# Kernel tuning notes

Hardware: AMD Instinct MI355X
Metric: run time of the kernel (lower is better)

Reference implementation:

```python
import jax, jax.numpy as jnp
import numpy as np

EPS = 1e-12  # matches torch F.normalize eps


def _l2_normalize(x):
    n = jnp.linalg.norm(x, axis=-1, keepdims=True)
    return x / jnp.maximum(n, EPS)


def setup_inputs() -> dict:
    key = jax.random.key(0)
    k1, k2, k3 = jax.random.split(key, 3)
    N, E, D = 100000, 1200000, 64
    feat = jax.random.normal(k1, (N, D), dtype=jnp.float32)
    beta = jnp.ones((1,), dtype=jnp.float32)
    src = jax.random.randint(k2, (E,), 0, N, dtype=jnp.int32)
    dst = jax.random.randint(k3, (E,), 0, N, dtype=jnp.int32)
    return {"feat": feat, "beta": beta, "src": src, "dst": dst}


def reference(feat, beta, src, dst):
    N = feat.shape[0]
    # cosine similarity on each edge (AGNN att_type)
    nh = _l2_normalize(feat)                                  # [N, D]
    e = beta[0] * jnp.sum(nh[src] * nh[dst], axis=-1)         # [E]
    # edge softmax over incoming edges of each destination node
    emax = jax.ops.segment_max(e, dst, num_segments=N)        # [N]
    emax = jnp.where(jnp.isfinite(emax), emax, 0.0)           # isolated nodes
    p = jnp.exp(e - emax[dst])                                # [E]
    psum = jax.ops.segment_sum(p, dst, num_segments=N)        # [N]
    p = p / jnp.maximum(psum[dst], EPS)                       # [E]
    # weighted scatter-sum aggregation: h_i' = sum_j p_ij * h_j
    msg = feat[src] * p[:, None]                              # [E, D]
    out = jax.ops.segment_sum(msg, dst, num_segments=N)       # [N, D]
    return out
```

## Files before the change

### kernel.cpp

```cpp
#include <hip/hip_runtime.h>
#include <hip/hip_fp16.h>

#define D 64
#define EPS 1e-12f
#define NPB 512
#define NPB_SHIFT 9
#define NB 256
#define CAP 8192
#define CAP_SHIFT 13
#define EPB 4096
#define SRC_BITS 17

typedef _Float16 hv2 __attribute__((ext_vector_type(2)));

__device__ inline unsigned bc_u(__half2 h) { return __builtin_bit_cast(unsigned, h); }
__device__ inline __half2  bc_h(unsigned u) { return __builtin_bit_cast(__half2, u); }

__device__ inline float fdot2f(unsigned a, unsigned b, float c) {
#if defined(__has_builtin) && __has_builtin(__builtin_amdgcn_fdot2)
    return __builtin_amdgcn_fdot2(__builtin_bit_cast(hv2, a),
                                  __builtin_bit_cast(hv2, b), c, false);
#else
    __half2 ah = bc_h(a), bh = bc_h(b);
    return c + __low2float(ah) * __low2float(bh)
             + __high2float(ah) * __high2float(bh);
#endif
}

__global__ __launch_bounds__(1024) void prep_scatter_kernel(
        const float4* __restrict__ feat4,
        float* __restrict__ norms,
        uint2* __restrict__ nh2,
        const int* __restrict__ src,
        const int* __restrict__ dst,
        int* __restrict__ bincursor,
        unsigned* __restrict__ pairs,
        int N, int E, int BI) {
    __shared__ int hist[NB], offs[NB], cursor[NB], gbase[NB], tmp[NB];
    __shared__ int dstbuf[EPB];
    __shared__ unsigned buf[EPB];
    __shared__ unsigned char binof[EPB];

    if ((int)blockIdx.x < BI) {
        int gid = blockIdx.x * 1024 + threadIdx.x;
        int row = gid >> 4;
        int lg  = gid & 15;
        if (row >= N) return;
        float4 v = feat4[row * 16 + lg];
        float ss = v.x * v.x + v.y * v.y + v.z * v.z + v.w * v.w;
        #pragma unroll
        for (int off = 1; off < 16; off <<= 1) ss += __shfl_xor(ss, off, 64);
        float nrm = fmaxf(sqrtf(ss), EPS);
        float inv = 1.0f / nrm;
        if (lg == 0) norms[row] = nrm;
        uint2 p;
        p.x = bc_u(__floats2half2_rn(v.x * inv, v.y * inv));
        p.y = bc_u(__floats2half2_rn(v.z * inv, v.w * inv));
        nh2[row * 16 + lg] = p;
        return;
    }

    int tid  = threadIdx.x;
    int base = (blockIdx.x - BI) * EPB;
    int cnt  = min(EPB, E - base);

    if (tid < NB) hist[tid] = 0;
    __syncthreads();
    for (int i = tid; i < cnt; i += 1024) {
        int dd = dst[base + i];
        dstbuf[i] = dd;
        atomicAdd(&hist[dd >> NPB_SHIFT], 1);
    }
    __syncthreads();
    int v = 0;
    if (tid < NB) { v = hist[tid]; tmp[tid] = v; }
    __syncthreads();
    #pragma unroll
    for (int off = 1; off < NB; off <<= 1) {
        int t = 0;
        if (tid < NB && tid >= off) t = tmp[tid - off];
        __syncthreads();
        if (tid < NB) tmp[tid] += t;
        __syncthreads();
    }
    if (tid < NB) {
        int e = tmp[tid] - v;
        offs[tid] = e; cursor[tid] = e;
        if (v > 0)
            gbase[tid] = (tid << CAP_SHIFT) + atomicAdd(&bincursor[tid], v);
    }
    __syncthreads();
    for (int i = tid; i < cnt; i += 1024) {
        int s = src[base + i], dd = dstbuf[i];
        int b = dd >> NPB_SHIFT;
        int l = atomicAdd(&cursor[b], 1);
        buf[l]   = ((unsigned)(dd & (NPB - 1)) << SRC_BITS) | (unsigned)s;
        binof[l] = (unsigned char)b;
    }
    __syncthreads();
    for (int i = tid; i < cnt; i += 1024) {
        int b = binof[i];
        pairs[gbase[b] + (i - offs[b])] = buf[i];
    }
}

__global__ __launch_bounds__(1024) void csr_kernel(const unsigned* __restrict__ pairs,
                                                   const int* __restrict__ bincursor,
                                                   int* __restrict__ rowbeg,
                                                   int* __restrict__ rowend,
                                                   int* __restrict__ esrc, int N) {
    __shared__ unsigned buf[CAP];
    __shared__ int hist[NPB], cursor[NPB], tmp[NPB];
    int b    = blockIdx.x;
    int tid  = threadIdx.x;
    int base = b << CAP_SHIFT;
    int cnt  = bincursor[b];
    int node0 = b << NPB_SHIFT;

    if (tid < NPB) hist[tid] = 0;
    __syncthreads();
    for (int i = tid; i < cnt; i += 1024) {
        unsigned p = pairs[base + i];
        buf[i] = p;
        atomicAdd(&hist[p >> SRC_BITS], 1);
    }
    __syncthreads();
    int v = 0;
    if (tid < NPB) { v = hist[tid]; tmp[tid] = v; }
    __syncthreads();
    #pragma unroll
    for (int off = 1; off < NPB; off <<= 1) {
        int t = 0;
        if (tid < NPB && tid >= off) t = tmp[tid - off];
        __syncthreads();
        if (tid < NPB) tmp[tid] += t;
        __syncthreads();
    }
    if (tid < NPB) {
        int excl = tmp[tid] - v;
        cursor[tid] = excl;
        int node = node0 + tid;
        if (node < N) { rowbeg[node] = base + excl; rowend[node] = base + excl + v; }
    }
    __syncthreads();
    for (int i = tid; i < cnt; i += 1024) {
        unsigned p = buf[i];
        int pos = atomicAdd(&cursor[p >> SRC_BITS], 1);
        esrc[base + pos] = (int)(p & ((1u << SRC_BITS) - 1));
    }
}

__global__ __launch_bounds__(256) void gather_kernel(const uint4* __restrict__ nh4,
                                                     const float* __restrict__ norms,
                                                     const float* __restrict__ beta_p,
                                                     const int* __restrict__ rowbeg,
                                                     const int* __restrict__ rowend,
                                                     const int* __restrict__ esrc,
                                                     float4* __restrict__ out4, int N) {
    int t    = blockIdx.x * 256 + threadIdx.x;
    int lane = threadIdx.x & 63;
    int g    = lane >> 3;
    int lg   = lane & 7;
    int d    = (t >> 6) * 8 + g;
    if (d >= N) return;

    int j   = rowbeg[d];
    int end = rowend[d];
    float beta = beta_p[0];

    uint4 fdp = nh4[(size_t)d * 8 + lg];

    __half2 acc0 = __float2half2_rn(0.f), acc1 = acc0, acc2 = acc0, acc3 = acc0;
    float ps = 0.f;

    for (; j < end; j += 2) {
        bool vb = (j + 1 < end);
        int  sa = esrc[j];
        int  sb = vb ? esrc[j + 1] : sa;
        uint4 pa = nh4[(size_t)sa * 8 + lg];
        uint4 pb = nh4[(size_t)sb * 8 + lg];
        float nsa = norms[sa], nsb = norms[sb];
        float dpa = fdot2f(pa.x, fdp.x, 0.f);
        float dpb = fdot2f(pb.x, fdp.x, 0.f);
        dpa = fdot2f(pa.y, fdp.y, dpa);  dpb = fdot2f(pb.y, fdp.y, dpb);
        dpa = fdot2f(pa.z, fdp.z, dpa);  dpb = fdot2f(pb.z, fdp.z, dpb);
        dpa = fdot2f(pa.w, fdp.w, dpa);  dpb = fdot2f(pb.w, fdp.w, dpb);
        #pragma unroll
        for (int off = 1; off < 8; off <<= 1) {
            dpa += __shfl_xor(dpa, off, 64);
            dpb += __shfl_xor(dpb, off, 64);
        }
        float wa = __expf(beta * dpa);
        float wb = vb ? __expf(beta * dpb) : 0.f;
        __half2 wa2 = __float2half2_rn(wa * nsa);
        __half2 wb2 = __float2half2_rn(wb * nsb);
        acc0 = __hfma2(wa2, bc_h(pa.x), acc0); acc0 = __hfma2(wb2, bc_h(pb.x), acc0);
        acc1 = __hfma2(wa2, bc_h(pa.y), acc1); acc1 = __hfma2(wb2, bc_h(pb.y), acc1);
        acc2 = __hfma2(wa2, bc_h(pa.z), acc2); acc2 = __hfma2(wb2, bc_h(pb.z), acc2);
        acc3 = __hfma2(wa2, bc_h(pa.w), acc3); acc3 = __hfma2(wb2, bc_h(pb.w), acc3);
        ps += wa + wb;
    }

    float r = 1.0f / fmaxf(ps, EPS);
    float4 o0 = {__low2float(acc0) * r, __high2float(acc0) * r,
                 __low2float(acc1) * r, __high2float(acc1) * r};
    float4 o1 = {__low2float(acc2) * r, __high2float(acc2) * r,
                 __low2float(acc3) * r, __high2float(acc3) * r};
    out4[(size_t)d * 16 + lg * 2]     = o0;
    out4[(size_t)d * 16 + lg * 2 + 1] = o1;
}

extern "C" void kernel_launch(void* const* d_in, const int* in_sizes, int n_in,
                              void* d_out, int out_size, void* d_ws, size_t ws_size,
                              hipStream_t stream) {
    const float* feat = (const float*)d_in[0];
    const float* beta = (const float*)d_in[1];
    const int*   src  = (const int*)d_in[2];
    const int*   dst  = (const int*)d_in[3];

    int N = in_sizes[0] / D;
    int E = in_sizes[2];
    int nbins = (N + NPB - 1) / NPB;

    unsigned* pairs     = (unsigned*)d_ws;
    int*      esrc      = (int*)(pairs + (size_t)nbins * CAP);
    unsigned* nhraw     = (unsigned*)(esrc + (size_t)nbins * CAP);
    float*    norms     = (float*)(nhraw + (size_t)N * 32);
    int*      bincursor = (int*)(norms + N);
    int*      rowbeg    = bincursor + NB;
    int*      rowend    = rowbeg + N;

    hipMemsetAsync(bincursor, 0, NB * sizeof(int), stream);

    int BI = (N * 16 + 1023) / 1024;
    int BS = (E + EPB - 1) / EPB;
    prep_scatter_kernel<<<BI + BS, 1024, 0, stream>>>(
        (const float4*)feat, norms, (uint2*)nhraw, src, dst, bincursor,
        pairs, N, E, BI);
    csr_kernel<<<nbins, 1024, 0, stream>>>(pairs, bincursor, rowbeg, rowend,
                                           esrc, N);
    gather_kernel<<<(N + 31) / 32, 256, 0, stream>>>(
        (const uint4*)nhraw, norms, beta, rowbeg, rowend, esrc,
        (float4*)d_out, N);
}
```

Measured before the change: 140.7 us.

## Move normalization into CSR kernel and unroll gather loop by four

Moves the per-node normalize/fp16 pack work out of the scatter kernel and merges it into the CSR build kernel as extra blocks, so it runs alongside the small number (196) of heavy CSR blocks and fills otherwise idle CUs. It also unrolls the gather edge loop from two to four edges per iteration, putting more independent gathers in flight. The cost is higher register pressure in the gather kernel and extra wasted work on tail iterations when a node's degree is not a multiple of four.

Result: faster. 134.8 us (-4.2%).

```diff
diff --git a/kernel.cpp b/kernel.cpp
--- a/kernel.cpp
+++ b/kernel.cpp
@@ -27,22 +27,75 @@
 #endif
 }
 
-__global__ __launch_bounds__(1024) void prep_scatter_kernel(
-        const float4* __restrict__ feat4,
-        float* __restrict__ norms,
-        uint2* __restrict__ nh2,
+__global__ __launch_bounds__(1024) void scatter_kernel(
         const int* __restrict__ src,
         const int* __restrict__ dst,
         int* __restrict__ bincursor,
-        unsigned* __restrict__ pairs,
-        int N, int E, int BI) {
+        unsigned* __restrict__ pairs, int E) {
     __shared__ int hist[NB], offs[NB], cursor[NB], gbase[NB], tmp[NB];
     __shared__ int dstbuf[EPB];
     __shared__ unsigned buf[EPB];
     __shared__ unsigned char binof[EPB];
 
-    if ((int)blockIdx.x < BI) {
-        int gid = blockIdx.x * 1024 + threadIdx.x;
+    int tid  = threadIdx.x;
+    int base = blockIdx.x * EPB;
+    int cnt  = min(EPB, E - base);
+
+    if (tid < NB) hist[tid] = 0;
+    __syncthreads();
+    for (int i = tid; i < cnt; i += 1024) {
+        int dd = dst[base + i];
+        dstbuf[i] = dd;
+        atomicAdd(&hist[dd >> NPB_SHIFT], 1);
+    }
+    __syncthreads();
+    int v = 0;
+    if (tid < NB) { v = hist[tid]; tmp[tid] = v; }
+    __syncthreads();
+    #pragma unroll
+    for (int off = 1; off < NB; off <<= 1) {
+        int t = 0;
+        if (tid < NB && tid >= off) t = tmp[tid - off];
+        __syncthreads();
+        if (tid < NB) tmp[tid] += t;
+        __syncthreads();
+    }
+    if (tid < NB) {
+        int e = tmp[tid] - v;
+        offs[tid] = e; cursor[tid] = e;
+        if (v > 0)
+            gbase[tid] = (tid << CAP_SHIFT) + atomicAdd(&bincursor[tid], v);
+    }
+    __syncthreads();
+    for (int i = tid; i < cnt; i += 1024) {
+        int s = src[base + i], dd = dstbuf[i];
+        int b = dd >> NPB_SHIFT;
+        int l = atomicAdd(&cursor[b], 1);
+        buf[l]   = ((unsigned)(dd & (NPB - 1)) << SRC_BITS) | (unsigned)s;
+        binof[l] = (unsigned char)b;
+    }
+    __syncthreads();
+    for (int i = tid; i < cnt; i += 1024) {
+        int b = binof[i];
+        pairs[gbase[b] + (i - offs[b])] = buf[i];
+    }
+}
+
+__global__ __launch_bounds__(1024) void csr_nh_kernel(
+        const unsigned* __restrict__ pairs,
+        const int* __restrict__ bincursor,
+        int* __restrict__ rowbeg,
+        int* __restrict__ rowend,
+        int* __restrict__ esrc,
+        const float4* __restrict__ feat4,
+        float* __restrict__ norms,
+        uint2* __restrict__ nh2,
+        int N, int nbins) {
+    __shared__ unsigned buf[CAP];
+    __shared__ int hist[NPB], cursor[NPB], tmp[NPB];
+
+    if ((int)blockIdx.x >= nbins) {
+        int gid = (blockIdx.x - nbins) * 1024 + threadIdx.x;
         int row = gid >> 4;
         int lg  = gid & 15;
         if (row >= N) return;
@@ -60,57 +113,6 @@
         return;
     }
 
-    int tid  = threadIdx.x;
-    int base = (blockIdx.x - BI) * EPB;
-    int cnt  = min(EPB, E - base);
-
-    if (tid < NB) hist[tid] = 0;
-    __syncthreads();
-    for (int i = tid; i < cnt; i += 1024) {
-        int dd = dst[base + i];
-        dstbuf[i] = dd;
-        atomicAdd(&hist[dd >> NPB_SHIFT], 1);
-    }
-    __syncthreads();
-    int v = 0;
-    if (tid < NB) { v = hist[tid]; tmp[tid] = v; }
-    __syncthreads();
-    #pragma unroll
-    for (int off = 1; off < NB; off <<= 1) {
-        int t = 0;
-        if (tid < NB && tid >= off) t = tmp[tid - off];
-        __syncthreads();
-        if (tid < NB) tmp[tid] += t;
-        __syncthreads();
-    }
-    if (tid < NB) {
-        int e = tmp[tid] - v;
-        offs[tid] = e; cursor[tid] = e;
-        if (v > 0)
-            gbase[tid] = (tid << CAP_SHIFT) + atomicAdd(&bincursor[tid], v);
-    }
-    __syncthreads();
-    for (int i = tid; i < cnt; i += 1024) {
-        int s = src[base + i], dd = dstbuf[i];
-        int b = dd >> NPB_SHIFT;
-        int l = atomicAdd(&cursor[b], 1);
-        buf[l]   = ((unsigned)(dd & (NPB - 1)) << SRC_BITS) | (unsigned)s;
-        binof[l] = (unsigned char)b;
-    }
-    __syncthreads();
-    for (int i = tid; i < cnt; i += 1024) {
-        int b = binof[i];
-        pairs[gbase[b] + (i - offs[b])] = buf[i];
-    }
-}
-
-__global__ __launch_bounds__(1024) void csr_kernel(const unsigned* __restrict__ pairs,
-                                                   const int* __restrict__ bincursor,
-                                                   int* __restrict__ rowbeg,
-                                                   int* __restrict__ rowend,
-                                                   int* __restrict__ esrc, int N) {
-    __shared__ unsigned buf[CAP];
-    __shared__ int hist[NPB], cursor[NPB], tmp[NPB];
     int b    = blockIdx.x;
     int tid  = threadIdx.x;
     int base = b << CAP_SHIFT;
@@ -173,32 +175,49 @@
     __half2 acc0 = __float2half2_rn(0.f), acc1 = acc0, acc2 = acc0, acc3 = acc0;
     float ps = 0.f;
 
-    for (; j < end; j += 2) {
-        bool vb = (j + 1 < end);
-        int  sa = esrc[j];
-        int  sb = vb ? esrc[j + 1] : sa;
-        uint4 pa = nh4[(size_t)sa * 8 + lg];
-        uint4 pb = nh4[(size_t)sb * 8 + lg];
-        float nsa = norms[sa], nsb = norms[sb];
-        float dpa = fdot2f(pa.x, fdp.x, 0.f);
-        float dpb = fdot2f(pb.x, fdp.x, 0.f);
-        dpa = fdot2f(pa.y, fdp.y, dpa);  dpb = fdot2f(pb.y, fdp.y, dpb);
-        dpa = fdot2f(pa.z, fdp.z, dpa);  dpb = fdot2f(pb.z, fdp.z, dpb);
-        dpa = fdot2f(pa.w, fdp.w, dpa);  dpb = fdot2f(pb.w, fdp.w, dpb);
+    for (; j < end; j += 4) {
+        bool v1 = (j + 1 < end), v2 = (j + 2 < end), v3 = (j + 3 < end);
+        int s0 = esrc[j];
+        int s1 = v1 ? esrc[j + 1] : s0;
+        int s2 = v2 ? esrc[j + 2] : s0;
+        int s3 = v3 ? esrc[j + 3] : s0;
+        uint4 p0 = nh4[(size_t)s0 * 8 + lg];
+        uint4 p1 = nh4[(size_t)s1 * 8 + lg];
+        uint4 p2 = nh4[(size_t)s2 * 8 + lg];
+        uint4 p3 = nh4[(size_t)s3 * 8 + lg];
+        float n0 = norms[s0], n1 = norms[s1], n2 = norms[s2], n3 = norms[s3];
+        float d0 = fdot2f(p0.x, fdp.x, 0.f), d1 = fdot2f(p1.x, fdp.x, 0.f);
+        float d2 = fdot2f(p2.x, fdp.x, 0.f), d3 = fdot2f(p3.x, fdp.x, 0.f);
+        d0 = fdot2f(p0.y, fdp.y, d0); d1 = fdot2f(p1.y, fdp.y, d1);
+        d2 = fdot2f(p2.y, fdp.y, d2); d3 = fdot2f(p3.y, fdp.y, d3);
+        d0 = fdot2f(p0.z, fdp.z, d0); d1 = fdot2f(p1.z, fdp.z, d1);
+        d2 = fdot2f(p2.z, fdp.z, d2); d3 = fdot2f(p3.z, fdp.z, d3);
+        d0 = fdot2f(p0.w, fdp.w, d0); d1 = fdot2f(p1.w, fdp.w, d1);
+        d2 = fdot2f(p2.w, fdp.w, d2); d3 = fdot2f(p3.w, fdp.w, d3);
         #pragma unroll
         for (int off = 1; off < 8; off <<= 1) {
-            dpa += __shfl_xor(dpa, off, 64);
-            dpb += __shfl_xor(dpb, off, 64);
+            d0 += __shfl_xor(d0, off, 64);
+            d1 += __shfl_xor(d1, off, 64);
+            d2 += __shfl_xor(d2, off, 64);
+            d3 += __shfl_xor(d3, off, 64);
         }
-        float wa = __expf(beta * dpa);
-        float wb = vb ? __expf(beta * dpb) : 0.f;
-        __half2 wa2 = __float2half2_rn(wa * nsa);
-        __half2 wb2 = __float2half2_rn(wb * nsb);
-        acc0 = __hfma2(wa2, bc_h(pa.x), acc0); acc0 = __hfma2(wb2, bc_h(pb.x), acc0);
-        acc1 = __hfma2(wa2, bc_h(pa.y), acc1); acc1 = __hfma2(wb2, bc_h(pb.y), acc1);
-        acc2 = __hfma2(wa2, bc_h(pa.z), acc2); acc2 = __hfma2(wb2, bc_h(pb.z), acc2);
-        acc3 = __hfma2(wa2, bc_h(pa.w), acc3); acc3 = __hfma2(wb2, bc_h(pb.w), acc3);
-        ps += wa + wb;
+        float w0 = __expf(beta * d0);
+        float w1 = v1 ? __expf(beta * d1) : 0.f;
+        float w2 = v2 ? __expf(beta * d2) : 0.f;
+        float w3 = v3 ? __expf(beta * d3) : 0.f;
+        __half2 q0 = __float2half2_rn(w0 * n0);
+        __half2 q1 = __float2half2_rn(w1 * n1);
+        __half2 q2 = __float2half2_rn(w2 * n2);
+        __half2 q3 = __float2half2_rn(w3 * n3);
+        acc0 = __hfma2(q0, bc_h(p0.x), acc0); acc0 = __hfma2(q1, bc_h(p1.x), acc0);
+        acc0 = __hfma2(q2, bc_h(p2.x), acc0); acc0 = __hfma2(q3, bc_h(p3.x), acc0);
+        acc1 = __hfma2(q0, bc_h(p0.y), acc1); acc1 = __hfma2(q1, bc_h(p1.y), acc1);
+        acc1 = __hfma2(q2, bc_h(p2.y), acc1); acc1 = __hfma2(q3, bc_h(p3.y), acc1);
+        acc2 = __hfma2(q0, bc_h(p0.z), acc2); acc2 = __hfma2(q1, bc_h(p1.z), acc2);
+        acc2 = __hfma2(q2, bc_h(p2.z), acc2); acc2 = __hfma2(q3, bc_h(p3.z), acc2);
+        acc3 = __hfma2(q0, bc_h(p0.w), acc3); acc3 = __hfma2(q1, bc_h(p1.w), acc3);
+        acc3 = __hfma2(q2, bc_h(p2.w), acc3); acc3 = __hfma2(q3, bc_h(p3.w), acc3);
+        ps += w0 + w1 + w2 + w3;
     }
 
     float r = 1.0f / fmaxf(ps, EPS);
@@ -232,13 +251,12 @@
 
     hipMemsetAsync(bincursor, 0, NB * sizeof(int), stream);
 
+    int BS = (E + EPB - 1) / EPB;
     int BI = (N * 16 + 1023) / 1024;
-    int BS = (E + EPB - 1) / EPB;
-    prep_scatter_kernel<<<BI + BS, 1024, 0, stream>>>(
-        (const float4*)feat, norms, (uint2*)nhraw, src, dst, bincursor,
-        pairs, N, E, BI);
-    csr_kernel<<<nbins, 1024, 0, stream>>>(pairs, bincursor, rowbeg, rowend,
-                                           esrc, N);
+    scatter_kernel<<<BS, 1024, 0, stream>>>(src, dst, bincursor, pairs, E);
+    csr_nh_kernel<<<nbins + BI, 1024, 0, stream>>>(
+        pairs, bincursor, rowbeg, rowend, esrc,
+        (const float4*)feat, norms, (uint2*)nhraw, N, nbins);
     gather_kernel<<<(N + 31) / 32, 256, 0, stream>>>(
         (const uint4*)nhraw, norms, beta, rowbeg, rowend, esrc,
         (float4*)d_out, N);
```
